# Kernel tuning notes

Measured on AMD Instinct MI355X. Metric: run time of the kernel, lower is better.

The kernel has to match this reference:

```python
import jax, jax.numpy as jnp
import numpy as np

D = 768          # model dim (ViT-Base)
H = 12           # num heads
DH = 64          # head dim
DFF = 4 * D      # mlp hidden
SMAX = 1024      # max sequence length in the packed batch
LENS = np.array([1024, 896, 768, 640, 512, 448, 256, 64], dtype=np.int32)
TOTAL = int(LENS.sum())  # 4608
LN_EPS = 1e-6
NEG = -1e30


def _ln(x, w, b):
    mu = jnp.mean(x, axis=-1, keepdims=True)
    var = jnp.mean(jnp.square(x - mu), axis=-1, keepdims=True)
    return (x - mu) * jax.lax.rsqrt(var + LN_EPS) * w + b


def setup_inputs() -> dict:
    key = jax.random.key(0)
    ks = jax.random.split(key, 16)
    s = 0.02
    cu = jnp.asarray(np.concatenate([[0], np.cumsum(LENS)]).astype(np.int32))
    return {
        "x": jax.random.normal(ks[0], (TOTAL, D), jnp.float32),
        "norm1_w": jnp.ones((D,), jnp.float32),
        "norm1_b": jnp.zeros((D,), jnp.float32),
        "qkv_w": jax.random.normal(ks[1], (3 * D, D), jnp.float32) * s,
        "qkv_b": jnp.zeros((3 * D,), jnp.float32),
        "proj_w": jax.random.normal(ks[2], (D, D), jnp.float32) * s,
        "proj_b": jnp.zeros((D,), jnp.float32),
        "ls1_gamma": jax.random.normal(ks[3], (D,), jnp.float32) * 0.1,
        "norm2_w": jnp.ones((D,), jnp.float32),
        "norm2_b": jnp.zeros((D,), jnp.float32),
        "fc1_w": jax.random.normal(ks[4], (DFF, D), jnp.float32) * s,
        "fc1_b": jnp.zeros((DFF,), jnp.float32),
        "fc2_w": jax.random.normal(ks[5], (D, DFF), jnp.float32) * s,
        "fc2_b": jnp.zeros((D,), jnp.float32),
        "ls2_gamma": jax.random.normal(ks[6], (D,), jnp.float32) * 0.1,
        "cu_seqlens": cu,
    }


def reference(x, norm1_w, norm1_b, qkv_w, qkv_b, proj_w, proj_b, ls1_gamma,
              norm2_w, norm2_b, fc1_w, fc1_b, fc2_w, fc2_b, ls2_gamma,
              cu_seqlens):
    total = x.shape[0]
    B = cu_seqlens.shape[0] - 1
    tok = jnp.arange(total)
    seg = jnp.searchsorted(cu_seqlens[1:], tok, side="right")  # [Total]
    pos = tok - cu_seqlens[seg]                                 # [Total]
    lens = cu_seqlens[1:] - cu_seqlens[:-1]                     # [B]

    # --- attention branch ---
    xn = _ln(x, norm1_w, norm1_b)
    qkv = (xn @ qkv_w.T + qkv_b).reshape(total, 3, H, DH)
    q, k, v = qkv[:, 0], qkv[:, 1], qkv[:, 2]                   # [Total,H,DH]

    # pad packed ragged tokens to [B, SMAX, H, DH]
    def pad(t):
        return jnp.zeros((B, SMAX, H, DH), t.dtype).at[seg, pos].set(t)
    qp, kp, vp = pad(q), pad(k), pad(v)

    valid = jnp.arange(SMAX)[None, :] < lens[:, None]           # [B,SMAX]
    scores = jnp.einsum("bqhd,bkhd->bhqk", qp, kp) * (DH ** -0.5)
    scores = jnp.where(valid[:, None, None, :], scores, NEG)
    attn = jax.nn.softmax(scores, axis=-1)
    out = jnp.einsum("bhqk,bkhd->bqhd", attn, vp)
    out = out[seg, pos].reshape(total, D)                       # back to packed

    attn_out = out @ proj_w.T + proj_b
    x = x + ls1_gamma * attn_out

    # --- mlp branch ---
    xn2 = _ln(x, norm2_w, norm2_b)
    h = jax.nn.gelu(xn2 @ fc1_w.T + fc1_b, approximate=False)
    h = h @ fc2_w.T + fc2_b
    return x + ls2_gamma * h
```

## Files before the change

### kernel.cpp

```cpp
#include <hip/hip_runtime.h>
#include <hip/hip_bf16.h>
#include <stdint.h>

#define D 768
#define HEADS 12
#define DHEAD 64
#define DFF 3072
#define TOTAL 4608
#define NSEG 8

typedef __bf16 bf16;
typedef __bf16 bf16x8 __attribute__((ext_vector_type(8)));
typedef __bf16 bf16x4 __attribute__((ext_vector_type(4)));
typedef float f32x4 __attribute__((ext_vector_type(4)));

__device__ __forceinline__ void gld_lds16(const void* g, void* l) {
  __builtin_amdgcn_global_load_lds(
      (const __attribute__((address_space(1))) void*)g,
      (__attribute__((address_space(3))) void*)(uintptr_t)l, 16, 0, 0);
}

__global__ __launch_bounds__(256) void cvt_all_kernel(
    const float* __restrict__ a, const float* __restrict__ b,
    const float* __restrict__ c, const float* __restrict__ d,
    bf16* __restrict__ out, int nA, int nAB, int nABC, int nTot) {
  int i = blockIdx.x * blockDim.x + threadIdx.x;
  if (i >= nTot) return;
  const float* src;
  int j;
  if (i < nA) { src = a; j = i; }
  else if (i < nAB) { src = b; j = i - nA; }
  else if (i < nABC) { src = c; j = i - nAB; }
  else { src = d; j = i - nABC; }
  float4 v = ((const float4*)src)[j];
  bf16x4 o;
  o[0] = (bf16)v.x; o[1] = (bf16)v.y; o[2] = (bf16)v.z; o[3] = (bf16)v.w;
  ((bf16x4*)out)[i] = o;
}

__global__ __launch_bounds__(256) void ln_kernel(
    const float* __restrict__ x, const float* __restrict__ w,
    const float* __restrict__ b, bf16* __restrict__ out) {
  __shared__ float red[8];
  int row = blockIdx.x;
  const float* xr = x + (size_t)row * D;
  int t = threadIdx.x;
  float v[3];
  float s = 0.f, s2 = 0.f;
#pragma unroll
  for (int j = 0; j < 3; j++) {
    v[j] = xr[t + 256 * j];
    s += v[j]; s2 += v[j] * v[j];
  }
#pragma unroll
  for (int m = 1; m <= 32; m <<= 1) {
    s += __shfl_xor(s, m);
    s2 += __shfl_xor(s2, m);
  }
  int wave = t >> 6, lane = t & 63;
  if (lane == 0) { red[wave] = s; red[4 + wave] = s2; }
  __syncthreads();
  s = red[0] + red[1] + red[2] + red[3];
  s2 = red[4] + red[5] + red[6] + red[7];
  float mu = s * (1.f / 768.f);
  float var = s2 * (1.f / 768.f) - mu * mu;
  float rstd = rsqrtf(var + 1e-6f);
#pragma unroll
  for (int j = 0; j < 3; j++) {
    int c = t + 256 * j;
    out[(size_t)row * D + c] = (bf16)((v[j] - mu) * rstd * w[c] + b[c]);
  }
}

__device__ __forceinline__ float fast_gelu(float v) {
  float u = v * (0.7978845608f + 0.0356774081f * v * v);
  float e = exp2f(2.8853900818f * u);
  float th = 1.f - 2.f * __builtin_amdgcn_rcpf(1.f + e);
  return 0.5f * v * (1.f + th);
}

template <int MODE, int TN>
__global__ __launch_bounds__(256) void gemm_kernel(
    const bf16* __restrict__ A, const bf16* __restrict__ W,
    const float* __restrict__ bias, const float* __restrict__ res,
    const float* __restrict__ gamma, bf16* __restrict__ outb,
    float* __restrict__ outf, int N, int K) {
  constexpr int NJ = TN / 32;
  __shared__ __align__(16) bf16 As[2][128 * 32];
  __shared__ __align__(16) bf16 Bs[2][TN * 32];
  const int m0 = blockIdx.x * 128, n0 = blockIdx.y * TN;
  const int t = threadIdx.x, wave = t >> 6, lane = t & 63;
  const int quad = lane >> 4, l16 = lane & 15;
  const int wm = (wave & 1) * 64, wn = (wave >> 1) * (TN / 4 * 2);

  const bf16* gA = A + (size_t)(m0 + wave * 32 + (lane >> 2)) * K + (lane & 3) * 8;
  const bf16* gB = W + (size_t)(n0 + wave * (TN / 4) + (lane >> 2)) * K + (lane & 3) * 8;
  const int lbA = (wave * 32) * 32;
  const int lbB = (wave * (TN / 4)) * 32;

  gld_lds16(gA, &As[0][lbA]);
  gld_lds16(gA + (size_t)16 * K, &As[0][lbA + 16 * 32]);
  gld_lds16(gB, &Bs[0][lbB]);
  if (TN == 128) gld_lds16(gB + (size_t)16 * K, &Bs[0][lbB + 16 * 32]);
  gA += 32; gB += 32;

  f32x4 acc[4][NJ] = {};
  int cur = 0;
  for (int k0 = 0; k0 < K; k0 += 32) {
    __syncthreads();
    if (k0 + 32 < K) {
      const int nxt = cur ^ 1;
      gld_lds16(gA, &As[nxt][lbA]);
      gld_lds16(gA + (size_t)16 * K, &As[nxt][lbA + 16 * 32]);
      gld_lds16(gB, &Bs[nxt][lbB]);
      if (TN == 128) gld_lds16(gB + (size_t)16 * K, &Bs[nxt][lbB + 16 * 32]);
      gA += 32; gB += 32;
    }
    const bf16* as = As[cur];
    const bf16* bs = Bs[cur];
    bf16x8 af[4], bg[NJ];
#pragma unroll
    for (int i = 0; i < 4; i++)
      af[i] = *(const bf16x8*)&as[(wm + i * 16 + l16) * 32 + quad * 8];
#pragma unroll
    for (int j = 0; j < NJ; j++)
      bg[j] = *(const bf16x8*)&bs[(wn + j * 16 + l16) * 32 + quad * 8];
#pragma unroll
    for (int i = 0; i < 4; i++)
#pragma unroll
      for (int j = 0; j < NJ; j++)
        acc[i][j] = __builtin_amdgcn_mfma_f32_16x16x32_bf16(af[i], bg[j], acc[i][j], 0, 0, 0);
    cur ^= 1;
  }

#pragma unroll
  for (int i = 0; i < 4; i++)
#pragma unroll
    for (int j = 0; j < NJ; j++)
#pragma unroll
      for (int r = 0; r < 4; r++) {
        int row = m0 + wm + i * 16 + quad * 4 + r;
        int col = n0 + wn + j * 16 + l16;
        float v = acc[i][j][r] + bias[col];
        if (MODE == 0) {
          outb[(size_t)row * N + col] = (bf16)v;
        } else if (MODE == 1) {
          outf[(size_t)row * N + col] = res[(size_t)row * N + col] + gamma[col] * v;
        } else {
          outb[(size_t)row * N + col] = (bf16)fast_gelu(v);
        }
      }
}

__global__ __launch_bounds__(256) void attn_kernel(
    const bf16* __restrict__ qkv, const int* __restrict__ cu,
    bf16* __restrict__ attn) {
  __shared__ __align__(16) bf16 Ks[64][72];
  __shared__ __align__(16) bf16 VTs[64][64];

  const int qt = blockIdx.x, h = blockIdx.y;
  const int tok0 = qt * 64;
  int b = 0;
  while (cu[b + 1] <= tok0) b++;
  const int s0 = cu[b], S = cu[b + 1] - s0;

  const int t = threadIdx.x, wave = t >> 6, lane = t & 63;
  const int quad = lane >> 4, l16 = lane & 15;

  const size_t qrow = (size_t)(tok0 + wave * 16 + l16) * (3 * D) + h * 64;
  const bf16x8 bq0 = *(const bf16x8*)&qkv[qrow + quad * 8];
  const bf16x8 bq1 = *(const bf16x8*)&qkv[qrow + 32 + quad * 8];

  const int srow = t >> 2, sc0 = (t & 3) * 16;
  const size_t kbase = (size_t)(s0 + srow) * (3 * D) + h * 64 + sc0 + D;
  const int vr0 = (t & 15) * 4, vd0 = (t >> 4) * 4;
  const size_t vbase = (size_t)(s0 + vr0) * (3 * D) + h * 64 + vd0 + 2 * D;
  const int kB0 = ((vr0 >> 5) << 5) | (((vr0 >> 2) & 3) << 3) | (((vr0 >> 4) & 1) << 2);

  bf16x8 kr0 = *(const bf16x8*)&qkv[kbase];
  bf16x8 kr1 = *(const bf16x8*)&qkv[kbase + 8];
  bf16x4 vp[4];
#pragma unroll
  for (int i = 0; i < 4; i++)
    vp[i] = *(const bf16x4*)&qkv[vbase + (size_t)i * (3 * D)];

  f32x4 Oacc[4] = {};
  float li = 0.f;
  const float SC = 0.125f * 1.44269504089f;

  for (int kb = 0; kb < S; kb += 64) {
    __syncthreads();
    *(bf16x8*)&Ks[srow][sc0] = kr0;
    *(bf16x8*)&Ks[srow][sc0 + 8] = kr1;
#pragma unroll
    for (int j = 0; j < 4; j++) {
      int d = vd0 + j;
      bf16x4 w;
      w[0] = vp[0][j]; w[1] = vp[1][j]; w[2] = vp[2][j]; w[3] = vp[3][j];
      *(bf16x4*)&VTs[d][kB0 ^ ((d & 7) * 8)] = w;
    }
    __syncthreads();

    if (kb + 64 < S) {
      const size_t koff = kbase + (size_t)(kb + 64) * (3 * D);
      const size_t voff = vbase + (size_t)(kb + 64) * (3 * D);
      kr0 = *(const bf16x8*)&qkv[koff];
      kr1 = *(const bf16x8*)&qkv[koff + 8];
#pragma unroll
      for (int i = 0; i < 4; i++)
        vp[i] = *(const bf16x4*)&qkv[voff + (size_t)i * (3 * D)];
    }

    f32x4 sac[4];
#pragma unroll
    for (int nt = 0; nt < 4; nt++) {
      bf16x8 ak0 = *(const bf16x8*)&Ks[nt * 16 + l16][quad * 8];
      bf16x8 ak1 = *(const bf16x8*)&Ks[nt * 16 + l16][32 + quad * 8];
      f32x4 z = {};
      z = __builtin_amdgcn_mfma_f32_16x16x32_bf16(ak0, bq0, z, 0, 0, 0);
      sac[nt] = __builtin_amdgcn_mfma_f32_16x16x32_bf16(ak1, bq1, z, 0, 0, 0);
    }

    bf16x8 bv0, bv1;
    float ls = 0.f;
#pragma unroll
    for (int r = 0; r < 4; r++) {
      float e0 = exp2f(sac[0][r] * SC);
      float e1 = exp2f(sac[1][r] * SC);
      float e2 = exp2f(sac[2][r] * SC);
      float e3 = exp2f(sac[3][r] * SC);
      ls += (e0 + e1) + (e2 + e3);
      bv0[r] = (bf16)e0; bv0[4 + r] = (bf16)e1;
      bv1[r] = (bf16)e2; bv1[4 + r] = (bf16)e3;
    }
    li += ls;

    const int vsw = (l16 & 7) * 8;
#pragma unroll
    for (int dt = 0; dt < 4; dt++) {
      bf16x8 av0 = *(const bf16x8*)&VTs[dt * 16 + l16][(quad * 8) ^ vsw];
      bf16x8 av1 = *(const bf16x8*)&VTs[dt * 16 + l16][(32 + quad * 8) ^ vsw];
      Oacc[dt] = __builtin_amdgcn_mfma_f32_16x16x32_bf16(av0, bv0, Oacc[dt], 0, 0, 0);
      Oacc[dt] = __builtin_amdgcn_mfma_f32_16x16x32_bf16(av1, bv1, Oacc[dt], 0, 0, 0);
    }
  }

  li += __shfl_xor(li, 16);
  li += __shfl_xor(li, 32);
  const float inv = 1.f / li;

  __syncthreads();
  bf16(*Osh)[72] = (bf16(*)[72])Ks;
  const int orow = wave * 16 + l16;
#pragma unroll
  for (int dt = 0; dt < 4; dt++) {
    int dg = dt * 16 + quad * 4;
    bf16x4 w;
#pragma unroll
    for (int r = 0; r < 4; r++) w[r] = (bf16)(Oacc[dt][r] * inv);
    *(bf16x4*)&Osh[orow][dg ^ ((l16 & 7) * 8)] = w;
  }
  const int osw = (l16 & 7) * 8;
  bf16x8 o0 = *(const bf16x8*)&Osh[orow][(quad * 16) ^ osw];
  bf16x8 o1 = *(const bf16x8*)&Osh[orow][(quad * 16 + 8) ^ osw];
  const size_t obase = (size_t)(tok0 + orow) * D + h * 64 + quad * 16;
  *(bf16x8*)&attn[obase] = o0;
  *(bf16x8*)&attn[obase + 8] = o1;
}

extern "C" void kernel_launch(void* const* d_in, const int* in_sizes, int n_in,
                              void* d_out, int out_size, void* d_ws,
                              size_t ws_size, hipStream_t stream) {
  const float* x       = (const float*)d_in[0];
  const float* norm1_w = (const float*)d_in[1];
  const float* norm1_b = (const float*)d_in[2];
  const float* qkv_w   = (const float*)d_in[3];
  const float* qkv_b   = (const float*)d_in[4];
  const float* proj_w  = (const float*)d_in[5];
  const float* proj_b  = (const float*)d_in[6];
  const float* ls1     = (const float*)d_in[7];
  const float* norm2_w = (const float*)d_in[8];
  const float* norm2_b = (const float*)d_in[9];
  const float* fc1_w   = (const float*)d_in[10];
  const float* fc1_b   = (const float*)d_in[11];
  const float* fc2_w   = (const float*)d_in[12];
  const float* fc2_b   = (const float*)d_in[13];
  const float* ls2     = (const float*)d_in[14];
  const int*   cu      = (const int*)d_in[15];
  float* out = (float*)d_out;

  char* ws = (char*)d_ws;
  size_t off = 0;
  auto alloc = [&](size_t bytes) {
    void* p = ws + off;
    off += (bytes + 255) & ~(size_t)255;
    return p;
  };
  bf16* w_qkv  = (bf16*)alloc((size_t)3 * D * D * 2);
  bf16* w_proj = (bf16*)alloc((size_t)D * D * 2);
  bf16* w_fc1  = (bf16*)alloc((size_t)DFF * D * 2);
  bf16* w_fc2  = (bf16*)alloc((size_t)D * DFF * 2);
  bf16* xn     = (bf16*)alloc((size_t)TOTAL * D * 2);
  bf16* qkv    = (bf16*)alloc((size_t)TOTAL * 3 * D * 2);
  bf16* attnb  = (bf16*)alloc((size_t)TOTAL * D * 2);
  float* x1    = (float*)alloc((size_t)TOTAL * D * 4);
  bf16* hbuf   = qkv;

  {
    int nA   = 3 * D * D / 4;
    int nAB  = nA + D * D / 4;
    int nABC = nAB + DFF * D / 4;
    int nTot = nABC + D * DFF / 4;
    cvt_all_kernel<<<(nTot + 255) / 256, 256, 0, stream>>>(
        qkv_w, proj_w, fc1_w, fc2_w, w_qkv, nA, nAB, nABC, nTot);
  }

  ln_kernel<<<TOTAL, 256, 0, stream>>>(x, norm1_w, norm1_b, xn);

  dim3 g1(TOTAL / 128, (3 * D) / 128);
  gemm_kernel<0, 128><<<g1, 256, 0, stream>>>(xn, w_qkv, qkv_b, nullptr, nullptr,
                                              qkv, nullptr, 3 * D, D);

  dim3 ga(TOTAL / 64, HEADS);
  attn_kernel<<<ga, 256, 0, stream>>>(qkv, cu, attnb);

  dim3 g2(TOTAL / 128, D / 64);
  gemm_kernel<1, 64><<<g2, 256, 0, stream>>>(attnb, w_proj, proj_b, x, ls1,
                                             nullptr, x1, D, D);

  ln_kernel<<<TOTAL, 256, 0, stream>>>(x1, norm2_w, norm2_b, xn);

  dim3 g3(TOTAL / 128, DFF / 128);
  gemm_kernel<2, 128><<<g3, 256, 0, stream>>>(xn, w_fc1, fc1_b, nullptr, nullptr,
                                              hbuf, nullptr, DFF, D);

  dim3 g4(TOTAL / 128, D / 64);
  gemm_kernel<1, 64><<<g4, 256, 0, stream>>>(hbuf, w_fc2, fc2_b, x1, ls2, nullptr,
                                             out, D, DFF);
}
```

Measured before the change: 283.7 us.

## Add XOR-swizzled LDS layout, templated K-tile, and N-major block order in GEMMs

Templates the GEMM on the K-tile depth, using BK=64 for the proj and fc2 GEMMs so each barrier covers twice the MFMA work. Applies an XOR swizzle to the 16-byte column groups in LDS on both the async global-to-LDS writes and the fragment reads, to reduce LDS bank conflicts. Swaps the grid axes so consecutive blocks walk along N for the same A rows, which should improve L2 reuse of activation tiles. The cost is doubled LDS per block for BK=64, which may reduce occupancy.

```diff
diff --git a/kernel.cpp b/kernel.cpp
--- a/kernel.cpp
+++ b/kernel.cpp
@@ -79,57 +79,72 @@
   return 0.5f * v * (1.f + th);
 }
 
-template <int MODE, int TN>
+template <int MODE, int TN, int BK>
 __global__ __launch_bounds__(256) void gemm_kernel(
     const bf16* __restrict__ A, const bf16* __restrict__ W,
     const float* __restrict__ bias, const float* __restrict__ res,
     const float* __restrict__ gamma, bf16* __restrict__ outb,
     float* __restrict__ outf, int N, int K) {
   constexpr int NJ = TN / 32;
-  __shared__ __align__(16) bf16 As[2][128 * 32];
-  __shared__ __align__(16) bf16 Bs[2][TN * 32];
-  const int m0 = blockIdx.x * 128, n0 = blockIdx.y * TN;
+  constexpr int KH = BK / 32;
+  constexpr int CG = BK / 8;
+  constexpr int SH = (BK == 32) ? 1 : 0;
+  constexpr int LPR = BK / 8;
+  constexpr int RS = 64 / LPR;
+  constexpr int RB = TN / 4;
+  __shared__ __align__(16) bf16 As[2][128 * BK];
+  __shared__ __align__(16) bf16 Bs[2][TN * BK];
+  const int m0 = blockIdx.y * 128, n0 = blockIdx.x * TN;
   const int t = threadIdx.x, wave = t >> 6, lane = t & 63;
   const int quad = lane >> 4, l16 = lane & 15;
-  const int wm = (wave & 1) * 64, wn = (wave >> 1) * (TN / 4 * 2);
-
-  const bf16* gA = A + (size_t)(m0 + wave * 32 + (lane >> 2)) * K + (lane & 3) * 8;
-  const bf16* gB = W + (size_t)(n0 + wave * (TN / 4) + (lane >> 2)) * K + (lane & 3) * 8;
-  const int lbA = (wave * 32) * 32;
-  const int lbB = (wave * (TN / 4)) * 32;
-
-  gld_lds16(gA, &As[0][lbA]);
-  gld_lds16(gA + (size_t)16 * K, &As[0][lbA + 16 * 32]);
-  gld_lds16(gB, &Bs[0][lbB]);
-  if (TN == 128) gld_lds16(gB + (size_t)16 * K, &Bs[0][lbB + 16 * 32]);
-  gA += 32; gB += 32;
+  const int wm = (wave & 1) * 64, wn = (wave >> 1) * (TN / 2);
+
+  const int ar = lane / LPR, ac = lane % LPR;
+  const int acg = ac ^ (((wave * 32 + ar) >> SH) & (CG - 1));
+  const int bcg = ac ^ (((wave * RB + ar) >> SH) & (CG - 1));
+  const bf16* gA = A + (size_t)(m0 + wave * 32 + ar) * K + acg * 8;
+  const bf16* gB = W + (size_t)(n0 + wave * RB + ar) * K + bcg * 8;
+
+  auto stage = [&](int buf) {
+#pragma unroll
+    for (int n = 0; n < 32 / RS; n++)
+      gld_lds16(gA + (size_t)n * RS * K, &As[buf][(wave * 32 + n * RS) * BK]);
+#pragma unroll
+    for (int n = 0; n < RB / RS; n++)
+      gld_lds16(gB + (size_t)n * RS * K, &Bs[buf][(wave * RB + n * RS) * BK]);
+    gA += BK; gB += BK;
+  };
+
+  stage(0);
 
   f32x4 acc[4][NJ] = {};
   int cur = 0;
-  for (int k0 = 0; k0 < K; k0 += 32) {
+  for (int k0 = 0; k0 < K; k0 += BK) {
     __syncthreads();
-    if (k0 + 32 < K) {
-      const int nxt = cur ^ 1;
-      gld_lds16(gA, &As[nxt][lbA]);
-      gld_lds16(gA + (size_t)16 * K, &As[nxt][lbA + 16 * 32]);
-      gld_lds16(gB, &Bs[nxt][lbB]);
-      if (TN == 128) gld_lds16(gB + (size_t)16 * K, &Bs[nxt][lbB + 16 * 32]);
-      gA += 32; gB += 32;
-    }
+    if (k0 + BK < K) stage(cur ^ 1);
     const bf16* as = As[cur];
     const bf16* bs = Bs[cur];
-    bf16x8 af[4], bg[NJ];
-#pragma unroll
-    for (int i = 0; i < 4; i++)
-      af[i] = *(const bf16x8*)&as[(wm + i * 16 + l16) * 32 + quad * 8];
-#pragma unroll
-    for (int j = 0; j < NJ; j++)
-      bg[j] = *(const bf16x8*)&bs[(wn + j * 16 + l16) * 32 + quad * 8];
-#pragma unroll
-    for (int i = 0; i < 4; i++)
-#pragma unroll
-      for (int j = 0; j < NJ; j++)
-        acc[i][j] = __builtin_amdgcn_mfma_f32_16x16x32_bf16(af[i], bg[j], acc[i][j], 0, 0, 0);
+    bf16x8 af[KH][4], bg[KH][NJ];
+#pragma unroll
+    for (int kh = 0; kh < KH; kh++) {
+#pragma unroll
+      for (int i = 0; i < 4; i++) {
+        int R = wm + i * 16 + l16;
+        af[kh][i] = *(const bf16x8*)&as[R * BK + 8 * ((kh * 4 + quad) ^ ((R >> SH) & (CG - 1)))];
+      }
+#pragma unroll
+      for (int j = 0; j < NJ; j++) {
+        int R = wn + j * 16 + l16;
+        bg[kh][j] = *(const bf16x8*)&bs[R * BK + 8 * ((kh * 4 + quad) ^ ((R >> SH) & (CG - 1)))];
+      }
+    }
+#pragma unroll
+    for (int kh = 0; kh < KH; kh++)
+#pragma unroll
+      for (int i = 0; i < 4; i++)
+#pragma unroll
+        for (int j = 0; j < NJ; j++)
+          acc[i][j] = __builtin_amdgcn_mfma_f32_16x16x32_bf16(af[kh][i], bg[kh][j], acc[i][j], 0, 0, 0);
     cur ^= 1;
   }
 
@@ -317,24 +332,24 @@
 
   ln_kernel<<<TOTAL, 256, 0, stream>>>(x, norm1_w, norm1_b, xn);
 
-  dim3 g1(TOTAL / 128, (3 * D) / 128);
-  gemm_kernel<0, 128><<<g1, 256, 0, stream>>>(xn, w_qkv, qkv_b, nullptr, nullptr,
-                                              qkv, nullptr, 3 * D, D);
+  dim3 g1((3 * D) / 128, TOTAL / 128);
+  gemm_kernel<0, 128, 32><<<g1, 256, 0, stream>>>(xn, w_qkv, qkv_b, nullptr, nullptr,
+                                                  qkv, nullptr, 3 * D, D);
 
   dim3 ga(TOTAL / 64, HEADS);
   attn_kernel<<<ga, 256, 0, stream>>>(qkv, cu, attnb);
 
-  dim3 g2(TOTAL / 128, D / 64);
-  gemm_kernel<1, 64><<<g2, 256, 0, stream>>>(attnb, w_proj, proj_b, x, ls1,
-                                             nullptr, x1, D, D);
+  dim3 g2(D / 64, TOTAL / 128);
+  gemm_kernel<1, 64, 64><<<g2, 256, 0, stream>>>(attnb, w_proj, proj_b, x, ls1,
+                                                 nullptr, x1, D, D);
 
   ln_kernel<<<TOTAL, 256, 0, stream>>>(x1, norm2_w, norm2_b, xn);
 
-  dim3 g3(TOTAL / 128, DFF / 128);
-  gemm_kernel<2, 128><<<g3, 256, 0, stream>>>(xn, w_fc1, fc1_b, nullptr, nullptr,
-                                              hbuf, nullptr, DFF, D);
-
-  dim3 g4(TOTAL / 128, D / 64);
-  gemm_kernel<1, 64><<<g4, 256, 0, stream>>>(hbuf, w_fc2, fc2_b, x1, ls2, nullptr,
-                                             out, D, DFF);
-}
+  dim3 g3(DFF / 128, TOTAL / 128);
+  gemm_kernel<2, 128, 32><<<g3, 256, 0, stream>>>(xn, w_fc1, fc1_b, nullptr, nullptr,
+                                                  hbuf, nullptr, DFF, D);
+
+  dim3 g4(D / 64, TOTAL / 128);
+  gemm_kernel<1, 64, 64><<<g4, 256, 0, stream>>>(hbuf, w_fc2, fc2_b, x1, ls2, nullptr,
+                                                 out, D, DFF);
+}
```

New measurement: 280.9 us. About the same (-1.0%).
